# Optimization experiments

Measured on AMD Instinct MI355X. Metric: run time of the kernel, lower is better.

## Reference

```python
import jax, jax.numpy as jnp
import numpy as np

B = 4096
IN = 1723 * 6          # 10338
H = 1024
OUT = 24 * 3 * 3 + 10 + 3  # 229
EPS = 1e-5


def _bn(x, g, b):
    # BatchNorm1d training-mode forward: biased batch statistics
    mu = jnp.mean(x, axis=0)
    var = jnp.var(x, axis=0)
    return g * (x - mu) * jax.lax.rsqrt(var + EPS) + b


def _resblock(h, wa, ba, ga, bea, wb, bb, gb, beb):
    t = jax.nn.relu(_bn(h @ wa + ba, ga, bea))
    t = _bn(t @ wb + bb, gb, beb)
    return jax.nn.relu(h + t)


def setup_inputs() -> dict:
    key = jax.random.key(0)
    ks = jax.random.split(key, 16)
    s = 0.02
    inp = {"x": jax.random.normal(ks[0], (B, IN), dtype=jnp.float32)}
    # FCBlock(IN -> H): Linear + BN + ReLU
    inp["w1"] = jax.random.normal(ks[1], (IN, H), dtype=jnp.float32) * s
    inp["b1"] = jnp.zeros((H,), jnp.float32)
    inp["g1"] = jnp.ones((H,), jnp.float32)
    inp["be1"] = jnp.zeros((H,), jnp.float32)
    # two FCResBlocks (H -> H)
    for i, kk in zip((2, 3), (ks[2:4], ks[4:6])):
        inp[f"w{i}a"] = jax.random.normal(kk[0], (H, H), dtype=jnp.float32) * s
        inp[f"b{i}a"] = jnp.zeros((H,), jnp.float32)
        inp[f"g{i}a"] = jnp.ones((H,), jnp.float32)
        inp[f"be{i}a"] = jnp.zeros((H,), jnp.float32)
        inp[f"w{i}b"] = jax.random.normal(kk[1], (H, H), dtype=jnp.float32) * s
        inp[f"b{i}b"] = jnp.zeros((H,), jnp.float32)
        inp[f"g{i}b"] = jnp.ones((H,), jnp.float32)
        inp[f"be{i}b"] = jnp.zeros((H,), jnp.float32)
    # final Linear (H -> OUT)
    inp["w4"] = jax.random.normal(ks[6], (H, OUT), dtype=jnp.float32) * s
    inp["b4"] = jnp.zeros((OUT,), jnp.float32)
    return inp


def reference(x, w1, b1, g1, be1,
              w2a, b2a, g2a, be2a, w2b, b2b, g2b, be2b,
              w3a, b3a, g3a, be3a, w3b, b3b, g3b, be3b,
              w4, b4):
    batch = x.shape[0]
    h = jax.nn.relu(_bn(x @ w1 + b1, g1, be1))
    h = _resblock(h, w2a, b2a, g2a, be2a, w2b, b2b, g2b, be2b)
    h = _resblock(h, w3a, b3a, g3a, be3a, w3b, b3b, g3b, be3b)
    out = h @ w4 + b4                              # (B, 229)

    rotmat = out[:, :216].reshape(-1, 3, 3)        # (B*24, 3, 3)
    betas = out[:, 216:226]                        # (B, 10)
    camera = out[:, 226:]                          # (B, 3)

    # batched 3x3 SVD orthogonalization (replaces per-sample Python loop)
    U, S, Vh = jnp.linalg.svd(rotmat, full_matrices=False)
    R = U @ Vh
    # det computed under no_grad in original -> stop_gradient
    det = jax.lax.stop_gradient(jnp.linalg.det(R))[:, None, None]
    R = (R * det).reshape(batch, 24, 3, 3)
    return (R, betas, camera)
```

## Files before the change

kernel.cpp:

```cpp
#include <hip/hip_runtime.h>
#include <math.h>


typedef _Float16 half8 __attribute__((ext_vector_type(8)));
typedef _Float16 half4_t __attribute__((ext_vector_type(4)));
typedef float floatx4 __attribute__((ext_vector_type(4)));

#define LO_SCALE 4096.0f
#define LO_INV (1.0f / 4096.0f)
#define IN_C 10338
#define INP_C 10368

__device__ __forceinline__ void gld16(const _Float16* g, _Float16* l) {
  __builtin_amdgcn_global_load_lds(
      (const __attribute__((address_space(1))) void*)g,
      (__attribute__((address_space(3))) void*)l, 16, 0, 0);
}

template <int TAG, int NY>
__global__ __launch_bounds__(256, 2)
void gemm_sk(const _Float16* __restrict__ Ah, const _Float16* __restrict__ Al,
             const _Float16* __restrict__ Bh, const _Float16* __restrict__ Bl,
             float* __restrict__ Cp, int Kld, int Ncols, int Ks,
             size_t partStride) {
  __shared__ _Float16 sAh[2][4096], sAl[2][4096];
  __shared__ _Float16 sBh[2][4096], sBl[2][4096];
  const int tid = threadIdx.x;
  const int wv = tid >> 6, ln = tid & 63;
  const int ln15 = ln & 15, q = ln >> 4;
  const int wr = wv >> 1, wc = wv & 1;

  const int gid = blockIdx.x;
  const int slot = gid >> 3;
  const int yz = (gid & 7) + 8 * (slot & 1);
  const int bm0 = (slot >> 1) * 128;
  const int bn0 = (yz % NY) * 128;
  const int bz = yz / NY;
  const int k0 = bz * Ks;
  Cp += (size_t)bz * partStride;

  const int srow = ln >> 2;
  const int swzw = (ln & 3) ^ (srow & 3) ^ ((srow >> 2) & 3);
  const int ch0 = wv * 2, ch1 = wv * 2 + 1;
  const size_t offA0 = (size_t)(bm0 + ch0 * 16 + srow) * Kld + k0 + swzw * 8;
  const size_t offA1 = (size_t)(bm0 + ch1 * 16 + srow) * Kld + k0 + swzw * 8;
  const size_t offB0 = (size_t)(bn0 + ch0 * 16 + srow) * Kld + k0 + swzw * 8;
  const size_t offB1 = (size_t)(bn0 + ch1 * 16 + srow) * Kld + k0 + swzw * 8;

  const int swzr = (q ^ (ln15 & 3) ^ ((ln15 >> 2) & 3)) * 8;
  const int aoff = (wr * 64 + ln15) * 32 + swzr;
  const int boff = (wc * 64 + ln15) * 32 + swzr;

  floatx4 acc[4][4];
  floatx4 acc2[4][4];
#pragma unroll
  for (int i = 0; i < 4; ++i)
#pragma unroll
    for (int j = 0; j < 4; ++j) {
      acc[i][j] = (floatx4){0.f, 0.f, 0.f, 0.f};
      acc2[i][j] = (floatx4){0.f, 0.f, 0.f, 0.f};
    }

  auto stage = [&](int kt, int buf) {
    gld16(Ah + offA0 + kt, &sAh[buf][ch0 * 512]);
    gld16(Ah + offA1 + kt, &sAh[buf][ch1 * 512]);
    gld16(Al + offA0 + kt, &sAl[buf][ch0 * 512]);
    gld16(Al + offA1 + kt, &sAl[buf][ch1 * 512]);
    gld16(Bh + offB0 + kt, &sBh[buf][ch0 * 512]);
    gld16(Bh + offB1 + kt, &sBh[buf][ch1 * 512]);
    gld16(Bl + offB0 + kt, &sBl[buf][ch0 * 512]);
    gld16(Bl + offB1 + kt, &sBl[buf][ch1 * 512]);
  };

  stage(0, 0);
  int cur = 0;
  for (int kt = 0; kt < Ks; kt += 32) {
    __syncthreads();
    if (kt + 32 < Ks) stage(kt + 32, cur ^ 1);

    const _Float16* pAh = &sAh[cur][aoff];
    const _Float16* pAl = &sAl[cur][aoff];
    const _Float16* pBh = &sBh[cur][boff];
    const _Float16* pBl = &sBl[cur][boff];
    half8 bh[4], bl[4];
#pragma unroll
    for (int ni = 0; ni < 4; ++ni) {
      bh[ni] = *(const half8*)(pBh + ni * 512);
      bl[ni] = *(const half8*)(pBl + ni * 512);
    }
#pragma unroll
    for (int mh = 0; mh < 2; ++mh) {
      half8 ah[2], al[2];
#pragma unroll
      for (int i = 0; i < 2; ++i) {
        ah[i] = *(const half8*)(pAh + (mh * 2 + i) * 512);
        al[i] = *(const half8*)(pAl + (mh * 2 + i) * 512);
      }
#pragma unroll
      for (int i = 0; i < 2; ++i) {
        const int mi = mh * 2 + i;
#pragma unroll
        for (int ni = 0; ni < 4; ++ni) {
          acc[mi][ni] = __builtin_amdgcn_mfma_f32_16x16x32_f16(
              ah[i], bh[ni], acc[mi][ni], 0, 0, 0);
          acc2[mi][ni] = __builtin_amdgcn_mfma_f32_16x16x32_f16(
              ah[i], bl[ni], acc2[mi][ni], 0, 0, 0);
          acc2[mi][ni] = __builtin_amdgcn_mfma_f32_16x16x32_f16(
              al[i], bh[ni], acc2[mi][ni], 0, 0, 0);
        }
      }
    }
    cur ^= 1;
  }

#pragma unroll
  for (int mi = 0; mi < 4; ++mi)
#pragma unroll
    for (int ni = 0; ni < 4; ++ni) {
      const int col = bn0 + wc * 64 + ni * 16 + ln15;
      const int rbase = bm0 + wr * 64 + mi * 16 + q * 4;
#pragma unroll
      for (int r = 0; r < 4; ++r)
        Cp[(size_t)(rbase + r) * Ncols + col] =
            acc[mi][ni][r] + acc2[mi][ni][r] * LO_INV;
    }
}

__global__ __launch_bounds__(256)
void split_pad_v(const float* __restrict__ X, _Float16* __restrict__ xh,
                 _Float16* __restrict__ xl, int total8) {
  int di = blockIdx.x * 256 + threadIdx.x;
  if (di >= total8) return;
  int base = di * 8;
  int row = base / INP_C;
  int col0 = base - row * INP_C;
  const float* src = X + (size_t)row * IN_C + col0;
  float v[8];
#pragma unroll
  for (int j = 0; j < 8; ++j) v[j] = (col0 + j < IN_C) ? src[j] : 0.f;
  half8 h, l;
#pragma unroll
  for (int j = 0; j < 8; ++j) {
    _Float16 hh = (_Float16)v[j];
    h[j] = hh;
    l[j] = (_Float16)((v[j] - (float)hh) * LO_SCALE);
  }
  *(half8*)(xh + base) = h;
  *(half8*)(xl + base) = l;
}

struct TJob {
  const float* src;
  _Float16* th;
  _Float16* tl;
  int K, N, Kpad, tK, start;
};
struct TJobs {
  TJob j[6];
};

__global__ __launch_bounds__(256)
void transpose_all(TJobs J) {
  const int b = blockIdx.x;
  int ji = 0;
#pragma unroll
  for (int i = 1; i < 6; ++i)
    if (b >= J.j[i].start) ji = i;
  const TJob job = J.j[ji];
  const int t = b - job.start;
  const int kk0 = (t % job.tK) * 32;
  const int nn0 = (t / job.tK) * 32;

  __shared__ float ts[32][33];
  const int tid = threadIdx.x;
  const int tx = tid & 31, ty = tid >> 5;
#pragma unroll
  for (int r = 0; r < 4; ++r) {
    int kk = kk0 + ty + r * 8;
    int nn = nn0 + tx;
    ts[ty + r * 8][tx] =
        (kk < job.K && nn < job.N) ? job.src[(size_t)kk * job.N + nn] : 0.f;
  }
  __syncthreads();
  const int tw = tid & 7, rw = tid >> 3;
  const int nn = nn0 + rw, kk = kk0 + tw * 4;
  half4_t h, l;
#pragma unroll
  for (int i2 = 0; i2 < 4; ++i2) {
    float v = ts[tw * 4 + i2][rw];
    _Float16 hh = (_Float16)v;
    h[i2] = hh;
    l[i2] = (_Float16)((v - (float)hh) * LO_SCALE);
  }
  size_t o = (size_t)nn * job.Kpad + kk;
  *(half4_t*)(job.th + o) = h;
  *(half4_t*)(job.tl + o) = l;
}

__global__ __launch_bounds__(256)
void reduce_bias_stats_v(const float* __restrict__ Cp,
                         const float* __restrict__ bias, float* __restrict__ Y,
                         float* __restrict__ psum, float* __restrict__ psq,
                         int S, size_t stride, int rowsPer) {
  const int N = 1024;
  const int t = threadIdx.x;
  const int cg = t & 15, rl = t >> 4;
  const int col4 = blockIdx.x * 64 + cg * 4;
  const int r0 = blockIdx.y * rowsPer;
  const floatx4 bs = *(const floatx4*)(bias + col4);
  floatx4 s = {0.f, 0.f, 0.f, 0.f}, qq = {0.f, 0.f, 0.f, 0.f};
  for (int r = r0 + rl; r < r0 + rowsPer; r += 16) {
    size_t i = (size_t)r * N + col4;
    floatx4 v = bs;
    for (int k = 0; k < S; ++k) v += *(const floatx4*)(Cp + k * stride + i);
    *(floatx4*)(Y + i) = v;
    s += v;
    qq += v * v;
  }
  __shared__ floatx4 ls[16][16], lq[16][16];
  ls[rl][cg] = s;
  lq[rl][cg] = qq;
  __syncthreads();
  if (t < 16) {
    floatx4 S4 = {0.f, 0.f, 0.f, 0.f}, Q4 = {0.f, 0.f, 0.f, 0.f};
#pragma unroll
    for (int r = 0; r < 16; ++r) {
      S4 += ls[r][t];
      Q4 += lq[r][t];
    }
    size_t o = (size_t)blockIdx.y * N + blockIdx.x * 64 + t * 4;
    *(floatx4*)(psum + o) = S4;
    *(floatx4*)(psq + o) = Q4;
  }
}

__global__ __launch_bounds__(256)
void bn_apply_v(const float* __restrict__ Y, const float* __restrict__ psum,
                const float* __restrict__ psq, const float* __restrict__ g,
                const float* __restrict__ be, const float* __restrict__ res,
                float* __restrict__ outf, _Float16* __restrict__ oh,
                _Float16* __restrict__ ol, int RB, float invM) {
  const int N = 1024;
  const int t = threadIdx.x;
  const int cg = t & 63, rl = t >> 6;
  const int col4 = blockIdx.x * 256 + cg * 4;
  __shared__ floatx4 lA[64], lB[64];
  if (t < 64) {
    int c4 = blockIdx.x * 256 + t * 4;
    floatx4 s = {0.f, 0.f, 0.f, 0.f}, qq = {0.f, 0.f, 0.f, 0.f};
    for (int rb = 0; rb < RB; ++rb) {
      s += *(const floatx4*)(psum + (size_t)rb * N + c4);
      qq += *(const floatx4*)(psq + (size_t)rb * N + c4);
    }
    floatx4 m = s * invM;
    floatx4 var = qq * invM - m * m;
    floatx4 rstd;
#pragma unroll
    for (int i = 0; i < 4; ++i) rstd[i] = rsqrtf(var[i] + 1e-5f);
    floatx4 a = (*(const floatx4*)(g + c4)) * rstd;
    lA[t] = a;
    lB[t] = (*(const floatx4*)(be + c4)) - m * a;
  }
  __syncthreads();
  const floatx4 a = lA[cg], b2 = lB[cg];
#pragma unroll
  for (int rr = 0; rr < 2; ++rr) {
    const int r = blockIdx.y * 8 + rl + rr * 4;
    const size_t i = (size_t)r * N + col4;
    floatx4 v = (*(const floatx4*)(Y + i)) * a + b2;
    if (res) v += *(const floatx4*)(res + i);
#pragma unroll
    for (int ii = 0; ii < 4; ++ii) v[ii] = fmaxf(v[ii], 0.f);
    if (outf) *(floatx4*)(outf + i) = v;
    half4_t h, l;
#pragma unroll
    for (int ii = 0; ii < 4; ++ii) {
      _Float16 hh = (_Float16)v[ii];
      h[ii] = hh;
      l[ii] = (_Float16)((v[ii] - (float)hh) * LO_SCALE);
    }
    *(half4_t*)(oh + i) = h;
    *(half4_t*)(ol + i) = l;
  }
}

__device__ __forceinline__ void cofactor3(const float X[9], float C[9]) {
  C[0] = X[4] * X[8] - X[5] * X[7];
  C[1] = X[5] * X[6] - X[3] * X[8];
  C[2] = X[3] * X[7] - X[4] * X[6];
  C[3] = X[2] * X[7] - X[1] * X[8];
  C[4] = X[0] * X[8] - X[2] * X[6];
  C[5] = X[1] * X[6] - X[0] * X[7];
  C[6] = X[1] * X[5] - X[2] * X[4];
  C[7] = X[2] * X[3] - X[0] * X[5];
  C[8] = X[0] * X[4] - X[1] * X[3];
}

__global__ __launch_bounds__(256)
void polar_tail(const float* __restrict__ Cp, const float* __restrict__ bias,
                float* __restrict__ out, int Bt, int nmat, int S,
                size_t stride) {
  const int ldy = 256;
  int idx = blockIdx.x * blockDim.x + threadIdx.x;
  if (idx < nmat) {
    int s = idx / 24, j = idx % 24;
    const size_t base = (size_t)s * ldy + j * 9;
    float A[9], X[9];
#pragma unroll
    for (int k = 0; k < 9; ++k) {
      float v = bias[j * 9 + k];
      for (int z = 0; z < S; ++z) v += Cp[z * stride + base + k];
      A[k] = v;
      X[k] = v;
    }
    double detA = (double)A[0] * ((double)A[4] * A[8] - (double)A[5] * A[7]) -
                  (double)A[1] * ((double)A[3] * A[8] - (double)A[5] * A[6]) +
                  (double)A[2] * ((double)A[3] * A[7] - (double)A[4] * A[6]);
    float sgn = (detA < 0.0) ? -1.f : 1.f;
#pragma unroll 1
    for (int it = 0; it < 12; ++it) {
      float C[9];
      cofactor3(X, C);
      float det = X[0] * C[0] + X[1] * C[1] + X[2] * C[2];
      float ad = fmaxf(fabsf(det), 1e-30f);
      float idet = (det < 0.f ? -1.f : 1.f) / ad;
      float n1 = 0.f, n2 = 0.f;
#pragma unroll
      for (int k = 0; k < 9; ++k) {
        n1 += X[k] * X[k];
        n2 += C[k] * C[k];
      }
      n1 = fmaxf(n1, 1e-30f);
      float zeta = sqrtf(sqrtf(n2 * idet * idet / n1));
      zeta = fminf(fmaxf(zeta, 1e-4f), 1e4f);
      float iz = 0.5f / zeta;
      float hz = 0.5f * zeta;
#pragma unroll
      for (int k = 0; k < 9; ++k) X[k] = hz * X[k] + iz * idet * C[k];
    }
    float* o = out + (size_t)idx * 9;
#pragma unroll
    for (int k = 0; k < 9; ++k) o[k] = X[k] * sgn;
  } else {
    int i = idx - nmat;
    int nb = Bt * 10;
    int nc = Bt * 3;
    int s, k, c;
    if (i < nb) {
      s = i / 10;
      k = i;
      c = 216 + (i % 10);
    } else if (i < nb + nc) {
      int t2 = i - nb;
      s = t2 / 3;
      k = i;
      c = 226 + (t2 % 3);
    } else {
      return;
    }
    float v = bias[c];
    size_t base = (size_t)s * ldy + c;
    for (int z = 0; z < S; ++z) v += Cp[z * stride + base];
    out[(size_t)Bt * 216 + k] = v;
  }
}

extern "C" void kernel_launch(void* const* d_in, const int* in_sizes, int n_in,
                              void* d_out, int out_size, void* d_ws,
                              size_t ws_size, hipStream_t stream) {
  const float* x = (const float*)d_in[0];
  const float* w1 = (const float*)d_in[1];
  const float* b1 = (const float*)d_in[2];
  const float* g1 = (const float*)d_in[3];
  const float* be1 = (const float*)d_in[4];
  const float* w2a = (const float*)d_in[5];
  const float* b2a = (const float*)d_in[6];
  const float* g2a = (const float*)d_in[7];
  const float* be2a = (const float*)d_in[8];
  const float* w2b = (const float*)d_in[9];
  const float* b2b = (const float*)d_in[10];
  const float* g2b = (const float*)d_in[11];
  const float* be2b = (const float*)d_in[12];
  const float* w3a = (const float*)d_in[13];
  const float* b3a = (const float*)d_in[14];
  const float* g3a = (const float*)d_in[15];
  const float* be3a = (const float*)d_in[16];
  const float* w3b = (const float*)d_in[17];
  const float* b3b = (const float*)d_in[18];
  const float* g3b = (const float*)d_in[19];
  const float* be3b = (const float*)d_in[20];
  const float* w4 = (const float*)d_in[21];
  const float* b4 = (const float*)d_in[22];
  float* out = (float*)d_out;

  const int B = 4096, IN = 10338, INP = 10368, H = 1024;
  const int OUTN = 229, OUTP = 256;
  const int RB = 32;
  const int S_BIG = 2, S_MID = 2, S_HEAD = 8;

  char* p = (char*)d_ws;
  auto alloc = [&](size_t bytes) -> void* {
    void* r = (void*)p;
    p += (bytes + 255) & ~(size_t)255;
    return r;
  };
  float* Cpart = (float*)alloc((size_t)S_HEAD * B * OUTP * 4);
  float* Y = (float*)alloc((size_t)B * H * 4);
  float* Hf = (float*)alloc((size_t)B * H * 4);
  _Float16* xh = (_Float16*)alloc((size_t)B * INP * 2);
  _Float16* xl = (_Float16*)alloc((size_t)B * INP * 2);
  _Float16* w1h = (_Float16*)alloc((size_t)H * INP * 2);
  _Float16* w1l = (_Float16*)alloc((size_t)H * INP * 2);
  _Float16 *wmh[4], *wml[4];
  for (int i = 0; i < 4; ++i) {
    wmh[i] = (_Float16*)alloc((size_t)H * H * 2);
    wml[i] = (_Float16*)alloc((size_t)H * H * 2);
  }
  _Float16* w4h = (_Float16*)alloc((size_t)OUTP * H * 2);
  _Float16* w4l = (_Float16*)alloc((size_t)OUTP * H * 2);
  _Float16* hh = (_Float16*)alloc((size_t)B * H * 2);
  _Float16* hl = (_Float16*)alloc((size_t)B * H * 2);
  float* psum = (float*)alloc((size_t)RB * H * 4);
  float* psq = (float*)alloc((size_t)RB * H * 4);

  {
    int total8 = B * INP / 8;
    split_pad_v<<<dim3((total8 + 255) / 256), 256, 0, stream>>>(x, xh, xl,
                                                                total8);
    TJobs J;
    const float* wsrc[6] = {w1, w2a, w2b, w3a, w3b, w4};
    _Float16* th[6] = {w1h, wmh[0], wmh[1], wmh[2], wmh[3], w4h};
    _Float16* tl[6] = {w1l, wml[0], wml[1], wml[2], wml[3], w4l};
    int Ks[6] = {IN, H, H, H, H, H};
    int Ns[6] = {H, H, H, H, H, OUTN};
    int Kpads[6] = {INP, H, H, H, H, H};
    int Npads[6] = {H, H, H, H, H, OUTP};
    int start = 0;
    for (int i = 0; i < 6; ++i) {
      J.j[i].src = wsrc[i];
      J.j[i].th = th[i];
      J.j[i].tl = tl[i];
      J.j[i].K = Ks[i];
      J.j[i].N = Ns[i];
      J.j[i].Kpad = Kpads[i];
      J.j[i].tK = Kpads[i] / 32;
      J.j[i].start = start;
      start += (Kpads[i] / 32) * (Npads[i] / 32);
    }
    transpose_all<<<dim3(start), 256, 0, stream>>>(J);
  }

  auto reducestats = [&](const float* bias, int S) {
    reduce_bias_stats_v<<<dim3(16, RB), 256, 0, stream>>>(
        Cpart, bias, Y, psum, psq, S, (size_t)B * H, B / RB);
  };
  auto bnapply = [&](const float* g, const float* be, const float* res,
                     float* outf) {
    bn_apply_v<<<dim3(H / 256, B / 8), 256, 0, stream>>>(
        Y, psum, psq, g, be, res, outf, hh, hl, RB, 1.f / B);
  };

  gemm_sk<0, 8><<<dim3(512), 256, 0, stream>>>(xh, xl, w1h, w1l, Cpart, INP, H,
                                               INP / S_BIG, (size_t)B * H);
  reducestats(b1, S_BIG);
  bnapply(g1, be1, nullptr, Hf);
  gemm_sk<1, 8><<<dim3(512), 256, 0, stream>>>(hh, hl, wmh[0], wml[0], Cpart,
                                               H, H, H / S_MID, (size_t)B * H);
  reducestats(b2a, S_MID);
  bnapply(g2a, be2a, nullptr, nullptr);
  gemm_sk<1, 8><<<dim3(512), 256, 0, stream>>>(hh, hl, wmh[1], wml[1], Cpart,
                                               H, H, H / S_MID, (size_t)B * H);
  reducestats(b2b, S_MID);
  bnapply(g2b, be2b, Hf, Hf);
  gemm_sk<1, 8><<<dim3(512), 256, 0, stream>>>(hh, hl, wmh[2], wml[2], Cpart,
                                               H, H, H / S_MID, (size_t)B * H);
  reducestats(b3a, S_MID);
  bnapply(g3a, be3a, nullptr, nullptr);
  gemm_sk<1, 8><<<dim3(512), 256, 0, stream>>>(hh, hl, wmh[3], wml[3], Cpart,
                                               H, H, H / S_MID, (size_t)B * H);
  reducestats(b3b, S_MID);
  bnapply(g3b, be3b, Hf, Hf);
  gemm_sk<2, 2><<<dim3(512), 256, 0, stream>>>(hh, hl, w4h, w4l, Cpart, H,
                                               OUTP, H / S_HEAD,
                                               (size_t)B * OUTP);

  int nmat = B * 24;
  int ntot = nmat + B * 13;
  polar_tail<<<dim3((ntot + 255) / 256), 256, 0, stream>>>(
      Cpart, b4, out, B, nmat, S_HEAD, (size_t)B * OUTP);
}
```

Baseline: 956.5 us.

## Fuse reduce and BN apply via grid barrier, merge conversion kernels, simplify GEMM grid

Merges the split-K reduction with bias, the BN statistics and the BN apply into one kernel. It uses a global atomic counter as a grid-wide barrier between computing partial sums and applying the normalization, so the Y tensor is re-read while still hot and one launch per layer is saved. The input split and the weight transpose kernels are combined into a single launch. The GEMM drops its custom XCD-aware block swizzle for a plain 3D grid, which may change L2 locality. The grid barrier needs all 512 blocks resident at once, and the counters are only reset once per call.

Result: slower. 1.189 ms (+24.3%).

```diff
diff --git a/kernel.cpp b/kernel.cpp
--- a/kernel.cpp
+++ b/kernel.cpp
@@ -17,7 +17,7 @@
       (__attribute__((address_space(3))) void*)l, 16, 0, 0);
 }
 
-template <int TAG, int NY>
+template <int TAG>
 __global__ __launch_bounds__(256, 2)
 void gemm_sk(const _Float16* __restrict__ Ah, const _Float16* __restrict__ Al,
              const _Float16* __restrict__ Bh, const _Float16* __restrict__ Bl,
@@ -29,15 +29,9 @@
   const int wv = tid >> 6, ln = tid & 63;
   const int ln15 = ln & 15, q = ln >> 4;
   const int wr = wv >> 1, wc = wv & 1;
-
-  const int gid = blockIdx.x;
-  const int slot = gid >> 3;
-  const int yz = (gid & 7) + 8 * (slot & 1);
-  const int bm0 = (slot >> 1) * 128;
-  const int bn0 = (yz % NY) * 128;
-  const int bz = yz / NY;
-  const int k0 = bz * Ks;
-  Cp += (size_t)bz * partStride;
+  const int bm0 = blockIdx.x * 128, bn0 = blockIdx.y * 128;
+  const int k0 = blockIdx.z * Ks;
+  Cp += (size_t)blockIdx.z * partStride;
 
   const int srow = ln >> 2;
   const int swzw = (ln & 3) ^ (srow & 3) ^ ((srow >> 2) & 3);
@@ -126,42 +120,44 @@
     }
 }
 
-__global__ __launch_bounds__(256)
-void split_pad_v(const float* __restrict__ X, _Float16* __restrict__ xh,
-                 _Float16* __restrict__ xl, int total8) {
-  int di = blockIdx.x * 256 + threadIdx.x;
-  if (di >= total8) return;
-  int base = di * 8;
-  int row = base / INP_C;
-  int col0 = base - row * INP_C;
-  const float* src = X + (size_t)row * IN_C + col0;
-  float v[8];
-#pragma unroll
-  for (int j = 0; j < 8; ++j) v[j] = (col0 + j < IN_C) ? src[j] : 0.f;
-  half8 h, l;
-#pragma unroll
-  for (int j = 0; j < 8; ++j) {
-    _Float16 hh = (_Float16)v[j];
-    h[j] = hh;
-    l[j] = (_Float16)((v[j] - (float)hh) * LO_SCALE);
-  }
-  *(half8*)(xh + base) = h;
-  *(half8*)(xl + base) = l;
-}
-
 struct TJob {
   const float* src;
   _Float16* th;
   _Float16* tl;
   int K, N, Kpad, tK, start;
 };
-struct TJobs {
+struct CJobs {
   TJob j[6];
+  const float* x;
+  _Float16* xh;
+  _Float16* xl;
+  int splitStart;
 };
 
 __global__ __launch_bounds__(256)
-void transpose_all(TJobs J) {
+void convert_all(CJobs J) {
   const int b = blockIdx.x;
+  const int tid = threadIdx.x;
+  if (b >= J.splitStart) {
+    int di = (b - J.splitStart) * 256 + tid;
+    int base = di * 8;
+    int row = base / INP_C;
+    int col0 = base - row * INP_C;
+    const float* src = J.x + (size_t)row * IN_C + col0;
+    float v[8];
+#pragma unroll
+    for (int j = 0; j < 8; ++j) v[j] = (col0 + j < IN_C) ? src[j] : 0.f;
+    half8 h, l;
+#pragma unroll
+    for (int j = 0; j < 8; ++j) {
+      _Float16 hh = (_Float16)v[j];
+      h[j] = hh;
+      l[j] = (_Float16)((v[j] - (float)hh) * LO_SCALE);
+    }
+    *(half8*)(J.xh + base) = h;
+    *(half8*)(J.xl + base) = l;
+    return;
+  }
   int ji = 0;
 #pragma unroll
   for (int i = 1; i < 6; ++i)
@@ -172,7 +168,6 @@
   const int nn0 = (t / job.tK) * 32;
 
   __shared__ float ts[32][33];
-  const int tid = threadIdx.x;
   const int tx = tid & 31, ty = tid >> 5;
 #pragma unroll
   for (int r = 0; r < 4; ++r) {
@@ -198,18 +193,23 @@
 }
 
 __global__ __launch_bounds__(256)
-void reduce_bias_stats_v(const float* __restrict__ Cp,
-                         const float* __restrict__ bias, float* __restrict__ Y,
-                         float* __restrict__ psum, float* __restrict__ psq,
-                         int S, size_t stride, int rowsPer) {
+void reduce_bn_fused(const float* __restrict__ Cp,
+                     const float* __restrict__ bias, const float* __restrict__ g,
+                     const float* __restrict__ be, const float* __restrict__ res,
+                     float* __restrict__ outf, _Float16* __restrict__ oh,
+                     _Float16* __restrict__ ol, float* __restrict__ Y,
+                     float* __restrict__ psum, float* __restrict__ psq, int S,
+                     size_t stride, int* __restrict__ counter, float invM) {
   const int N = 1024;
   const int t = threadIdx.x;
   const int cg = t & 15, rl = t >> 4;
-  const int col4 = blockIdx.x * 64 + cg * 4;
-  const int r0 = blockIdx.y * rowsPer;
+  const int cb = blockIdx.x, rb = blockIdx.y;
+  const int col4 = cb * 64 + cg * 4;
+  const int r0 = rb * 128;
+
   const floatx4 bs = *(const floatx4*)(bias + col4);
   floatx4 s = {0.f, 0.f, 0.f, 0.f}, qq = {0.f, 0.f, 0.f, 0.f};
-  for (int r = r0 + rl; r < r0 + rowsPer; r += 16) {
+  for (int r = r0 + rl; r < r0 + 128; r += 16) {
     size_t i = (size_t)r * N + col4;
     floatx4 v = bs;
     for (int k = 0; k < S; ++k) v += *(const floatx4*)(Cp + k * stride + i);
@@ -228,45 +228,55 @@
       S4 += ls[r][t];
       Q4 += lq[r][t];
     }
-    size_t o = (size_t)blockIdx.y * N + blockIdx.x * 64 + t * 4;
+    size_t o = (size_t)rb * N + cb * 64 + t * 4;
     *(floatx4*)(psum + o) = S4;
     *(floatx4*)(psq + o) = Q4;
   }
-}
-
-__global__ __launch_bounds__(256)
-void bn_apply_v(const float* __restrict__ Y, const float* __restrict__ psum,
-                const float* __restrict__ psq, const float* __restrict__ g,
-                const float* __restrict__ be, const float* __restrict__ res,
-                float* __restrict__ outf, _Float16* __restrict__ oh,
-                _Float16* __restrict__ ol, int RB, float invM) {
-  const int N = 1024;
-  const int t = threadIdx.x;
-  const int cg = t & 63, rl = t >> 6;
-  const int col4 = blockIdx.x * 256 + cg * 4;
-  __shared__ floatx4 lA[64], lB[64];
-  if (t < 64) {
-    int c4 = blockIdx.x * 256 + t * 4;
-    floatx4 s = {0.f, 0.f, 0.f, 0.f}, qq = {0.f, 0.f, 0.f, 0.f};
-    for (int rb = 0; rb < RB; ++rb) {
-      s += *(const floatx4*)(psum + (size_t)rb * N + c4);
-      qq += *(const floatx4*)(psq + (size_t)rb * N + c4);
-    }
-    floatx4 m = s * invM;
-    floatx4 var = qq * invM - m * m;
+  __threadfence();
+  __syncthreads();
+  if (t == 0) {
+    __hip_atomic_fetch_add(counter, 1, __ATOMIC_ACQ_REL,
+                           __HIP_MEMORY_SCOPE_AGENT);
+    while (__hip_atomic_load(counter, __ATOMIC_ACQUIRE,
+                             __HIP_MEMORY_SCOPE_AGENT) < 512)
+      __builtin_amdgcn_s_sleep(8);
+  }
+  __syncthreads();
+
+  {
+    const int cc = cb * 64 + (t & 15) * 4;
+    const int pr = t >> 4;
+    floatx4 S4 = *(const floatx4*)(psum + (size_t)pr * N + cc);
+    S4 += *(const floatx4*)(psum + (size_t)(pr + 16) * N + cc);
+    floatx4 Q4 = *(const floatx4*)(psq + (size_t)pr * N + cc);
+    Q4 += *(const floatx4*)(psq + (size_t)(pr + 16) * N + cc);
+    ls[pr][t & 15] = S4;
+    lq[pr][t & 15] = Q4;
+  }
+  __syncthreads();
+  __shared__ floatx4 lA[16], lB[16];
+  if (t < 16) {
+    floatx4 S4 = {0.f, 0.f, 0.f, 0.f}, Q4 = {0.f, 0.f, 0.f, 0.f};
+#pragma unroll
+    for (int r = 0; r < 16; ++r) {
+      S4 += ls[r][t];
+      Q4 += lq[r][t];
+    }
+    floatx4 m = S4 * invM;
+    floatx4 var = Q4 * invM - m * m;
     floatx4 rstd;
 #pragma unroll
     for (int i = 0; i < 4; ++i) rstd[i] = rsqrtf(var[i] + 1e-5f);
-    floatx4 a = (*(const floatx4*)(g + c4)) * rstd;
+    const int cc = cb * 64 + t * 4;
+    floatx4 a = (*(const floatx4*)(g + cc)) * rstd;
     lA[t] = a;
-    lB[t] = (*(const floatx4*)(be + c4)) - m * a;
-  }
-  __syncthreads();
+    lB[t] = (*(const floatx4*)(be + cc)) - m * a;
+  }
+  __syncthreads();
+
   const floatx4 a = lA[cg], b2 = lB[cg];
-#pragma unroll
-  for (int rr = 0; rr < 2; ++rr) {
-    const int r = blockIdx.y * 8 + rl + rr * 4;
-    const size_t i = (size_t)r * N + col4;
+  for (int r = r0 + rl; r < r0 + 128; r += 16) {
+    size_t i = (size_t)r * N + col4;
     floatx4 v = (*(const floatx4*)(Y + i)) * a + b2;
     if (res) v += *(const floatx4*)(res + i);
 #pragma unroll
@@ -395,7 +405,6 @@
 
   const int B = 4096, IN = 10338, INP = 10368, H = 1024;
   const int OUTN = 229, OUTP = 256;
-  const int RB = 32;
   const int S_BIG = 2, S_MID = 2, S_HEAD = 8;
 
   char* p = (char*)d_ws;
@@ -420,14 +429,14 @@
   _Float16* w4l = (_Float16*)alloc((size_t)OUTP * H * 2);
   _Float16* hh = (_Float16*)alloc((size_t)B * H * 2);
   _Float16* hl = (_Float16*)alloc((size_t)B * H * 2);
-  float* psum = (float*)alloc((size_t)RB * H * 4);
-  float* psq = (float*)alloc((size_t)RB * H * 4);
+  float* psum = (float*)alloc((size_t)32 * H * 4);
+  float* psq = (float*)alloc((size_t)32 * H * 4);
+  int* counters = (int*)alloc(8 * sizeof(int));
+
+  hipMemsetAsync(counters, 0, 8 * sizeof(int), stream);
 
   {
-    int total8 = B * INP / 8;
-    split_pad_v<<<dim3((total8 + 255) / 256), 256, 0, stream>>>(x, xh, xl,
-                                                                total8);
-    TJobs J;
+    CJobs J;
     const float* wsrc[6] = {w1, w2a, w2b, w3a, w3b, w4};
     _Float16* th[6] = {w1h, wmh[0], wmh[1], wmh[2], wmh[3], w4h};
     _Float16* tl[6] = {w1l, wml[0], wml[1], wml[2], wml[3], w4l};
@@ -447,42 +456,39 @@
       J.j[i].start = start;
       start += (Kpads[i] / 32) * (Npads[i] / 32);
     }
-    transpose_all<<<dim3(start), 256, 0, stream>>>(J);
-  }
-
-  auto reducestats = [&](const float* bias, int S) {
-    reduce_bias_stats_v<<<dim3(16, RB), 256, 0, stream>>>(
-        Cpart, bias, Y, psum, psq, S, (size_t)B * H, B / RB);
+    J.x = x;
+    J.xh = xh;
+    J.xl = xl;
+    J.splitStart = start;
+    int total = start + (B * INP / 8 + 255) / 256;
+    convert_all<<<dim3(total), 256, 0, stream>>>(J);
+  }
+
+  auto reducebn = [&](const float* bias, int S, const float* g,
+                      const float* be, const float* res, float* outf,
+                      int layer) {
+    reduce_bn_fused<<<dim3(16, 32), 256, 0, stream>>>(
+        Cpart, bias, g, be, res, outf, hh, hl, Y, psum, psq, S, (size_t)B * H,
+        counters + layer, 1.f / B);
   };
-  auto bnapply = [&](const float* g, const float* be, const float* res,
-                     float* outf) {
-    bn_apply_v<<<dim3(H / 256, B / 8), 256, 0, stream>>>(
-        Y, psum, psq, g, be, res, outf, hh, hl, RB, 1.f / B);
-  };
-
-  gemm_sk<0, 8><<<dim3(512), 256, 0, stream>>>(xh, xl, w1h, w1l, Cpart, INP, H,
-                                               INP / S_BIG, (size_t)B * H);
-  reducestats(b1, S_BIG);
-  bnapply(g1, be1, nullptr, Hf);
-  gemm_sk<1, 8><<<dim3(512), 256, 0, stream>>>(hh, hl, wmh[0], wml[0], Cpart,
-                                               H, H, H / S_MID, (size_t)B * H);
-  reducestats(b2a, S_MID);
-  bnapply(g2a, be2a, nullptr, nullptr);
-  gemm_sk<1, 8><<<dim3(512), 256, 0, stream>>>(hh, hl, wmh[1], wml[1], Cpart,
-                                               H, H, H / S_MID, (size_t)B * H);
-  reducestats(b2b, S_MID);
-  bnapply(g2b, be2b, Hf, Hf);
-  gemm_sk<1, 8><<<dim3(512), 256, 0, stream>>>(hh, hl, wmh[2], wml[2], Cpart,
-                                               H, H, H / S_MID, (size_t)B * H);
-  reducestats(b3a, S_MID);
-  bnapply(g3a, be3a, nullptr, nullptr);
-  gemm_sk<1, 8><<<dim3(512), 256, 0, stream>>>(hh, hl, wmh[3], wml[3], Cpart,
-                                               H, H, H / S_MID, (size_t)B * H);
-  reducestats(b3b, S_MID);
-  bnapply(g3b, be3b, Hf, Hf);
-  gemm_sk<2, 2><<<dim3(512), 256, 0, stream>>>(hh, hl, w4h, w4l, Cpart, H,
-                                               OUTP, H / S_HEAD,
-                                               (size_t)B * OUTP);
+
+  gemm_sk<0><<<dim3(B / 128, H / 128, S_BIG), 256, 0, stream>>>(
+      xh, xl, w1h, w1l, Cpart, INP, H, INP / S_BIG, (size_t)B * H);
+  reducebn(b1, S_BIG, g1, be1, nullptr, Hf, 0);
+  gemm_sk<1><<<dim3(B / 128, H / 128, S_MID), 256, 0, stream>>>(
+      hh, hl, wmh[0], wml[0], Cpart, H, H, H / S_MID, (size_t)B * H);
+  reducebn(b2a, S_MID, g2a, be2a, nullptr, nullptr, 1);
+  gemm_sk<1><<<dim3(B / 128, H / 128, S_MID), 256, 0, stream>>>(
+      hh, hl, wmh[1], wml[1], Cpart, H, H, H / S_MID, (size_t)B * H);
+  reducebn(b2b, S_MID, g2b, be2b, Hf, Hf, 2);
+  gemm_sk<1><<<dim3(B / 128, H / 128, S_MID), 256, 0, stream>>>(
+      hh, hl, wmh[2], wml[2], Cpart, H, H, H / S_MID, (size_t)B * H);
+  reducebn(b3a, S_MID, g3a, be3a, nullptr, nullptr, 3);
+  gemm_sk<1><<<dim3(B / 128, H / 128, S_MID), 256, 0, stream>>>(
+      hh, hl, wmh[3], wml[3], Cpart, H, H, H / S_MID, (size_t)B * H);
+  reducebn(b3b, S_MID, g3b, be3b, Hf, Hf, 4);
+  gemm_sk<2><<<dim3(B / 128, OUTP / 128, S_HEAD), 256, 0, stream>>>(
+      hh, hl, w4h, w4l, Cpart, H, OUTP, H / S_HEAD, (size_t)B * OUTP);
 
   int nmat = B * 24;
   int ntot = nmat + B * 13;
```

## Fuse bias and BN stats into mid GEMM epilogue, drop split-K, merge conversion kernels

Applied to the files above, without the earlier changes.

The four H×H GEMMs now run without split-K. Each writes Y directly, adds the bias and accumulates per-column sum and sum-of-squares through an LDS reduction, which removes the separate reduce_bias_stats pass and the partial-buffer traffic. The input split/pad kernel is merged into the weight-transpose launch to save a launch. The custom XCD-aware block swizzle is replaced by a plain 3D grid. This halves the block count for the mid GEMMs (256 blocks) and may lower occupancy or L2 locality.

After: 925.8 us. -3.2%, faster.

```diff
diff --git a/kernel.cpp b/kernel.cpp
--- a/kernel.cpp
+++ b/kernel.cpp
@@ -17,27 +17,22 @@
       (__attribute__((address_space(3))) void*)l, 16, 0, 0);
 }
 
-template <int TAG, int NY>
+template <int TAG, bool STATS>
 __global__ __launch_bounds__(256, 2)
 void gemm_sk(const _Float16* __restrict__ Ah, const _Float16* __restrict__ Al,
              const _Float16* __restrict__ Bh, const _Float16* __restrict__ Bl,
              float* __restrict__ Cp, int Kld, int Ncols, int Ks,
-             size_t partStride) {
+             size_t partStride, const float* __restrict__ bias,
+             float* __restrict__ psum, float* __restrict__ psq) {
   __shared__ _Float16 sAh[2][4096], sAl[2][4096];
   __shared__ _Float16 sBh[2][4096], sBl[2][4096];
   const int tid = threadIdx.x;
   const int wv = tid >> 6, ln = tid & 63;
   const int ln15 = ln & 15, q = ln >> 4;
   const int wr = wv >> 1, wc = wv & 1;
-
-  const int gid = blockIdx.x;
-  const int slot = gid >> 3;
-  const int yz = (gid & 7) + 8 * (slot & 1);
-  const int bm0 = (slot >> 1) * 128;
-  const int bn0 = (yz % NY) * 128;
-  const int bz = yz / NY;
-  const int k0 = bz * Ks;
-  Cp += (size_t)bz * partStride;
+  const int bm0 = blockIdx.x * 128, bn0 = blockIdx.y * 128;
+  const int k0 = blockIdx.z * Ks;
+  Cp += (size_t)blockIdx.z * partStride;
 
   const int srow = ln >> 2;
   const int swzw = (ln & 3) ^ (srow & 3) ^ ((srow >> 2) & 3);
@@ -113,6 +108,14 @@
     cur ^= 1;
   }
 
+  float bs[4];
+  float sacc[4] = {0.f, 0.f, 0.f, 0.f};
+  float qacc[4] = {0.f, 0.f, 0.f, 0.f};
+  if constexpr (STATS) {
+#pragma unroll
+    for (int ni = 0; ni < 4; ++ni)
+      bs[ni] = bias[bn0 + wc * 64 + ni * 16 + ln15];
+  }
 #pragma unroll
   for (int mi = 0; mi < 4; ++mi)
 #pragma unroll
@@ -120,33 +123,39 @@
       const int col = bn0 + wc * 64 + ni * 16 + ln15;
       const int rbase = bm0 + wr * 64 + mi * 16 + q * 4;
 #pragma unroll
-      for (int r = 0; r < 4; ++r)
-        Cp[(size_t)(rbase + r) * Ncols + col] =
-            acc[mi][ni][r] + acc2[mi][ni][r] * LO_INV;
-    }
-}
-
-__global__ __launch_bounds__(256)
-void split_pad_v(const float* __restrict__ X, _Float16* __restrict__ xh,
-                 _Float16* __restrict__ xl, int total8) {
-  int di = blockIdx.x * 256 + threadIdx.x;
-  if (di >= total8) return;
-  int base = di * 8;
-  int row = base / INP_C;
-  int col0 = base - row * INP_C;
-  const float* src = X + (size_t)row * IN_C + col0;
-  float v[8];
-#pragma unroll
-  for (int j = 0; j < 8; ++j) v[j] = (col0 + j < IN_C) ? src[j] : 0.f;
-  half8 h, l;
-#pragma unroll
-  for (int j = 0; j < 8; ++j) {
-    _Float16 hh = (_Float16)v[j];
-    h[j] = hh;
-    l[j] = (_Float16)((v[j] - (float)hh) * LO_SCALE);
-  }
-  *(half8*)(xh + base) = h;
-  *(half8*)(xl + base) = l;
+      for (int r = 0; r < 4; ++r) {
+        float v = acc[mi][ni][r] + acc2[mi][ni][r] * LO_INV;
+        if constexpr (STATS) {
+          v += bs[ni];
+          sacc[ni] += v;
+          qacc[ni] += v * v;
+        }
+        Cp[(size_t)(rbase + r) * Ncols + col] = v;
+      }
+    }
+  if constexpr (STATS) {
+    __syncthreads();
+    float* sS = (float*)&sAh[0][0];
+    float* sQ = (float*)&sAl[0][0];
+    const int contrib = wr * 4 + q;
+#pragma unroll
+    for (int ni = 0; ni < 4; ++ni) {
+      const int colt = wc * 64 + ni * 16 + ln15;
+      sS[contrib * 128 + colt] = sacc[ni];
+      sQ[contrib * 128 + colt] = qacc[ni];
+    }
+    __syncthreads();
+    if (tid < 128) {
+      float S = 0.f, Q = 0.f;
+#pragma unroll
+      for (int c = 0; c < 8; ++c) {
+        S += sS[c * 128 + tid];
+        Q += sQ[c * 128 + tid];
+      }
+      psum[(size_t)blockIdx.x * 1024 + bn0 + tid] = S;
+      psq[(size_t)blockIdx.x * 1024 + bn0 + tid] = Q;
+    }
+  }
 }
 
 struct TJob {
@@ -155,13 +164,38 @@
   _Float16* tl;
   int K, N, Kpad, tK, start;
 };
-struct TJobs {
+struct CJobs {
   TJob j[6];
+  const float* x;
+  _Float16* xh;
+  _Float16* xl;
+  int splitStart;
 };
 
 __global__ __launch_bounds__(256)
-void transpose_all(TJobs J) {
+void convert_all(CJobs J) {
   const int b = blockIdx.x;
+  const int tid = threadIdx.x;
+  if (b >= J.splitStart) {
+    int di = (b - J.splitStart) * 256 + tid;
+    int base = di * 8;
+    int row = base / INP_C;
+    int col0 = base - row * INP_C;
+    const float* src = J.x + (size_t)row * IN_C + col0;
+    float v[8];
+#pragma unroll
+    for (int j = 0; j < 8; ++j) v[j] = (col0 + j < IN_C) ? src[j] : 0.f;
+    half8 h, l;
+#pragma unroll
+    for (int j = 0; j < 8; ++j) {
+      _Float16 hh = (_Float16)v[j];
+      h[j] = hh;
+      l[j] = (_Float16)((v[j] - (float)hh) * LO_SCALE);
+    }
+    *(half8*)(J.xh + base) = h;
+    *(half8*)(J.xl + base) = l;
+    return;
+  }
   int ji = 0;
 #pragma unroll
   for (int i = 1; i < 6; ++i)
@@ -172,7 +206,6 @@
   const int nn0 = (t / job.tK) * 32;
 
   __shared__ float ts[32][33];
-  const int tid = threadIdx.x;
   const int tx = tid & 31, ty = tid >> 5;
 #pragma unroll
   for (int r = 0; r < 4; ++r) {
@@ -396,7 +429,7 @@
   const int B = 4096, IN = 10338, INP = 10368, H = 1024;
   const int OUTN = 229, OUTP = 256;
   const int RB = 32;
-  const int S_BIG = 2, S_MID = 2, S_HEAD = 8;
+  const int S_BIG = 2, S_HEAD = 8;
 
   char* p = (char*)d_ws;
   auto alloc = [&](size_t bytes) -> void* {
@@ -424,10 +457,7 @@
   float* psq = (float*)alloc((size_t)RB * H * 4);
 
   {
-    int total8 = B * INP / 8;
-    split_pad_v<<<dim3((total8 + 255) / 256), 256, 0, stream>>>(x, xh, xl,
-                                                                total8);
-    TJobs J;
+    CJobs J;
     const float* wsrc[6] = {w1, w2a, w2b, w3a, w3b, w4};
     _Float16* th[6] = {w1h, wmh[0], wmh[1], wmh[2], wmh[3], w4h};
     _Float16* tl[6] = {w1l, wml[0], wml[1], wml[2], wml[3], w4l};
@@ -447,42 +477,42 @@
       J.j[i].start = start;
       start += (Kpads[i] / 32) * (Npads[i] / 32);
     }
-    transpose_all<<<dim3(start), 256, 0, stream>>>(J);
-  }
-
-  auto reducestats = [&](const float* bias, int S) {
-    reduce_bias_stats_v<<<dim3(16, RB), 256, 0, stream>>>(
-        Cpart, bias, Y, psum, psq, S, (size_t)B * H, B / RB);
-  };
+    J.x = x;
+    J.xh = xh;
+    J.xl = xl;
+    J.splitStart = start;
+    int total = start + (B * INP / 8 + 255) / 256;
+    convert_all<<<dim3(total), 256, 0, stream>>>(J);
+  }
+
   auto bnapply = [&](const float* g, const float* be, const float* res,
                      float* outf) {
     bn_apply_v<<<dim3(H / 256, B / 8), 256, 0, stream>>>(
         Y, psum, psq, g, be, res, outf, hh, hl, RB, 1.f / B);
   };
-
-  gemm_sk<0, 8><<<dim3(512), 256, 0, stream>>>(xh, xl, w1h, w1l, Cpart, INP, H,
-                                               INP / S_BIG, (size_t)B * H);
-  reducestats(b1, S_BIG);
+  auto midgemm = [&](const _Float16* Bh, const _Float16* Bl,
+                     const float* bias) {
+    gemm_sk<1, true><<<dim3(B / 128, H / 128, 1), 256, 0, stream>>>(
+        hh, hl, Bh, Bl, Y, H, H, H, 0, bias, psum, psq);
+  };
+
+  gemm_sk<0, false><<<dim3(B / 128, H / 128, S_BIG), 256, 0, stream>>>(
+      xh, xl, w1h, w1l, Cpart, INP, H, INP / S_BIG, (size_t)B * H, nullptr,
+      nullptr, nullptr);
+  reduce_bias_stats_v<<<dim3(16, RB), 256, 0, stream>>>(
+      Cpart, b1, Y, psum, psq, S_BIG, (size_t)B * H, B / RB);
   bnapply(g1, be1, nullptr, Hf);
-  gemm_sk<1, 8><<<dim3(512), 256, 0, stream>>>(hh, hl, wmh[0], wml[0], Cpart,
-                                               H, H, H / S_MID, (size_t)B * H);
-  reducestats(b2a, S_MID);
+  midgemm(wmh[0], wml[0], b2a);
   bnapply(g2a, be2a, nullptr, nullptr);
-  gemm_sk<1, 8><<<dim3(512), 256, 0, stream>>>(hh, hl, wmh[1], wml[1], Cpart,
-                                               H, H, H / S_MID, (size_t)B * H);
-  reducestats(b2b, S_MID);
+  midgemm(wmh[1], wml[1], b2b);
   bnapply(g2b, be2b, Hf, Hf);
-  gemm_sk<1, 8><<<dim3(512), 256, 0, stream>>>(hh, hl, wmh[2], wml[2], Cpart,
-                                               H, H, H / S_MID, (size_t)B * H);
-  reducestats(b3a, S_MID);
+  midgemm(wmh[2], wml[2], b3a);
   bnapply(g3a, be3a, nullptr, nullptr);
-  gemm_sk<1, 8><<<dim3(512), 256, 0, stream>>>(hh, hl, wmh[3], wml[3], Cpart,
-                                               H, H, H / S_MID, (size_t)B * H);
-  reducestats(b3b, S_MID);
+  midgemm(wmh[3], wml[3], b3b);
   bnapply(g3b, be3b, Hf, Hf);
-  gemm_sk<2, 2><<<dim3(512), 256, 0, stream>>>(hh, hl, w4h, w4l, Cpart, H,
-                                               OUTP, H / S_HEAD,
-                                               (size_t)B * OUTP);
+  gemm_sk<2, false><<<dim3(B / 128, OUTP / 128, S_HEAD), 256, 0, stream>>>(
+      hh, hl, w4h, w4l, Cpart, H, OUTP, H / S_HEAD, (size_t)B * OUTP, nullptr,
+      nullptr, nullptr);
 
   int nmat = B * 24;
   int ntot = nmat + B * 13;
```
